# Kernel optimization log

Hardware: AMD Instinct MI355X
Metric: run time of the kernel (lower is better)

Reference implementation:

```python
import jax, jax.numpy as jnp
import numpy as np

NUM_HEADS = 16
FIELD_SIZE = 512
SIGMA = 3.0
EMB = 1024


def _causal_kernel_fft(G, sigma):
    # kernel[i] = exp(-|i - G//2| / sigma) for i < G//2, else 0; normalized
    i = np.arange(G)
    dist = np.abs(i - G // 2)
    kernel = np.where(i >= G // 2, 0.0, np.exp(-dist / sigma)).astype(np.float32)
    kernel = kernel / (kernel.sum() + 1e-8)
    return jnp.asarray(np.fft.rfft(kernel), dtype=jnp.complex64)


def setup_inputs() -> dict:
    key = jax.random.key(0)
    ks = jax.random.split(key, 9)
    B, N, D = 4, 4096, EMB
    s = 1.0 / np.sqrt(D)
    return {
        "x": jax.random.normal(ks[0], (B, N, D), dtype=jnp.float32),
        "q_w": jax.random.uniform(ks[1], (D, D), minval=-s, maxval=s, dtype=jnp.float32),
        "q_b": jnp.zeros((D,), jnp.float32),
        "k_w": jax.random.uniform(ks[2], (D, D), minval=-s, maxval=s, dtype=jnp.float32),
        "k_b": jnp.zeros((D,), jnp.float32),
        "v_w": jax.random.uniform(ks[3], (D, D), minval=-s, maxval=s, dtype=jnp.float32),
        "v_b": jnp.zeros((D,), jnp.float32),
        "out_w": jax.random.uniform(ks[4], (D, D), minval=-s, maxval=s, dtype=jnp.float32),
        "out_b": jnp.zeros((D,), jnp.float32),
    }


def reference(x, q_w, q_b, k_w, k_b, v_w, v_b, out_w, out_b):
    B, N, D = x.shape
    H, hd, G = NUM_HEADS, D // NUM_HEADS, FIELD_SIZE

    # projections (q is computed in the original but unused downstream)
    q = x @ q_w.T + q_b  # noqa: F841 (faithful to original)
    k = (x @ k_w.T + k_b).reshape(B, N, H, hd).transpose(0, 2, 1, 3)  # (B,H,N,hd)
    v = (x @ v_w.T + v_b).reshape(B, N, H, hd).transpose(0, 2, 1, 3)

    # map sequence positions -> field bins (same for all b, h)
    pos = jnp.arange(N, dtype=jnp.float32) / max(N - 1, 1) * (G - 1)
    field_idx = jnp.clip(pos.astype(jnp.int32), 0, G - 1)  # (N,)

    # weighted values by key magnitude
    k_mag = jnp.linalg.norm(k, axis=-1, keepdims=True)  # (B,H,N,1)
    wv = v * k_mag  # (B,H,N,hd)

    # scatter-add tokens into field bins (vectorized over B,H,hd)
    field = jax.ops.segment_sum(wv.transpose(2, 0, 1, 3), field_idx,
                                num_segments=G)  # (G,B,H,hd)
    field = field.transpose(1, 2, 0, 3)  # (B,H,G,hd)

    # causal convolution along the field via FFT (circular, as in original)
    kfft = _causal_kernel_fft(G, SIGMA)
    f_fft = jnp.fft.rfft(field, n=G, axis=2)
    conv = jnp.fft.irfft(f_fft * kfft[None, None, :, None], n=G, axis=2)

    # gather back to token positions
    out = conv[:, :, field_idx, :]  # (B,H,N,hd)
    out = out.transpose(0, 2, 1, 3).reshape(B, N, D)
    return out @ out_w.T + out_b
```

## Files before the change

kernel.cpp:

```cpp
#include <hip/hip_runtime.h>
#include <hip/hip_bf16.h>

#define NPOS 4096
#define DIM  1024
#define GSZ  512

#define GAS __attribute__((address_space(1)))
#define LAS __attribute__((address_space(3)))

typedef __attribute__((ext_vector_type(8))) short bf16x8;
typedef __attribute__((ext_vector_type(4))) float f32x4;

__device__ __forceinline__ void async_load16(const void* g, void* l) {
  __builtin_amdgcn_global_load_lds((const GAS void*)g, (LAS void*)l, 16, 0, 0);
}

__device__ __forceinline__ int fidx_of(int n) {
  return (int)(((float)n / 4095.0f) * 511.0f);
}

__device__ __forceinline__ float bf2f(unsigned short s) {
  union { unsigned u; float f; } v; v.u = ((unsigned)s) << 16; return v.f;
}

__global__ __launch_bounds__(256) void cast_f32_to_bf16(
    const float* __restrict__ src, __hip_bfloat16* __restrict__ dst, int n) {
  int i = (blockIdx.x * 256 + threadIdx.x) * 4;
  if (i < n) {
    float4 f = *(const float4*)(src + i);
    ushort4 o;
    __hip_bfloat16 t;
    t = __float2bfloat16(f.x); o.x = *(unsigned short*)&t;
    t = __float2bfloat16(f.y); o.y = *(unsigned short*)&t;
    t = __float2bfloat16(f.z); o.z = *(unsigned short*)&t;
    t = __float2bfloat16(f.w); o.w = *(unsigned short*)&t;
    *(ushort4*)(dst + i) = o;
  }
}

template<bool OUTBF16>
__global__ __launch_bounds__(256) void gemm_bt(
    const __hip_bfloat16* __restrict__ A,
    const __hip_bfloat16* __restrict__ B,
    const float* __restrict__ bias0, const float* __restrict__ bias1,
    void* __restrict__ Cv, int N) {
  const int K = 1024;
  __shared__ __align__(16) __hip_bfloat16 As[128 * 32];
  __shared__ __align__(16) __hip_bfloat16 Bs[128 * 32];
  const int tid = threadIdx.x;
  const int bm = blockIdx.x * 128, bn = blockIdx.y * 128;

  const int srow = tid >> 2;
  const int scol = (tid & 3) * 8;
  const __hip_bfloat16* ap0 = A + (size_t)(bm + srow) * K + scol;
  const __hip_bfloat16* ap1 = A + (size_t)(bm + srow + 64) * K + scol;
  const __hip_bfloat16* bp0 = B + (size_t)(bn + srow) * K + scol;
  const __hip_bfloat16* bp1 = B + (size_t)(bn + srow + 64) * K + scol;
  __hip_bfloat16* as0 = &As[srow * 32 + scol];
  __hip_bfloat16* as1 = &As[(srow + 64) * 32 + scol];
  __hip_bfloat16* bs0 = &Bs[srow * 32 + scol];
  __hip_bfloat16* bs1 = &Bs[(srow + 64) * 32 + scol];

  const int wave = tid >> 6, lane = tid & 63;
  const int wm = (wave >> 1) * 64, wn = (wave & 1) * 64;
  const int m16 = lane & 15, quad = lane >> 4;

  f32x4 acc[4][4];
#pragma unroll
  for (int i = 0; i < 4; i++)
#pragma unroll
    for (int j = 0; j < 4; j++) acc[i][j] = (f32x4)0.f;

  for (int k0 = 0; k0 < K; k0 += 32) {
    async_load16(ap0 + k0, as0);
    async_load16(ap1 + k0, as1);
    async_load16(bp0 + k0, bs0);
    async_load16(bp1 + k0, bs1);
    __syncthreads();
    bf16x8 af[4], bfr[4];
#pragma unroll
    for (int mt = 0; mt < 4; mt++)
      af[mt] = *(const bf16x8*)&As[(wm + mt * 16 + m16) * 32 + quad * 8];
#pragma unroll
    for (int nt = 0; nt < 4; nt++)
      bfr[nt] = *(const bf16x8*)&Bs[(wn + nt * 16 + m16) * 32 + quad * 8];
#pragma unroll
    for (int mt = 0; mt < 4; mt++)
#pragma unroll
      for (int nt = 0; nt < 4; nt++)
        acc[mt][nt] = __builtin_amdgcn_mfma_f32_16x16x32_bf16(af[mt], bfr[nt], acc[mt][nt], 0, 0, 0);
    __syncthreads();
  }

#pragma unroll
  for (int mt = 0; mt < 4; mt++) {
#pragma unroll
    for (int nt = 0; nt < 4; nt++) {
      int col = bn + wn + nt * 16 + m16;
      float bv = (col < 1024) ? bias0[col] : bias1[col - 1024];
#pragma unroll
      for (int r = 0; r < 4; r++) {
        int row = bm + wm + mt * 16 + quad * 4 + r;
        float v = acc[mt][nt][r] + bv;
        if (OUTBF16)
          ((__hip_bfloat16*)Cv)[(size_t)row * N + col] = __float2bfloat16(v);
        else
          ((float*)Cv)[(size_t)row * N + col] = v;
      }
    }
  }
}

__global__ __launch_bounds__(256) void wv_field_kernel(
    const __hip_bfloat16* __restrict__ KV, float* __restrict__ field) {
  const int b = blockIdx.x, g = blockIdx.y;
  int i0 = (g * 4095 + 510) / 511;
  while (i0 > 0 && fidx_of(i0 - 1) >= g) --i0;
  while (i0 < NPOS && fidx_of(i0) < g) ++i0;
  int i1;
  if (g == GSZ - 1) i1 = NPOS;
  else {
    i1 = ((g + 1) * 4095 + 510) / 511;
    while (i1 > 0 && fidx_of(i1 - 1) >= g + 1) --i1;
    while (i1 < NPOS && fidx_of(i1) < g + 1) ++i1;
  }
  int cnt = i1 - i0;
  if (cnt > 12) cnt = 12;
  __shared__ float km[12][16];
  const int tid = threadIdx.x;
  if (tid < cnt * 16) {
    int r = tid >> 4, h = tid & 15;
    const unsigned short* kp = (const unsigned short*)KV + (size_t)(b * NPOS + i0 + r) * 2048 + h * 64;
    float s = 0.f;
#pragma unroll
    for (int e = 0; e < 64; e += 8) {
      bf16x8 v = *(const bf16x8*)(kp + e);
#pragma unroll
      for (int q = 0; q < 8; ++q) { float f = bf2f((unsigned short)v[q]); s += f * f; }
    }
    km[r][h] = sqrtf(s);
  }
  __syncthreads();
  if (tid < 128) {
    int c0 = tid * 8, h = c0 >> 6;
    float acc[8] = {0.f, 0.f, 0.f, 0.f, 0.f, 0.f, 0.f, 0.f};
    for (int r = 0; r < cnt; ++r) {
      float w = km[r][h];
      bf16x8 v = *(const bf16x8*)((const unsigned short*)KV + (size_t)(b * NPOS + i0 + r) * 2048 + 1024 + c0);
#pragma unroll
      for (int q = 0; q < 8; ++q) acc[q] += w * bf2f((unsigned short)v[q]);
    }
    float4* fp = (float4*)(field + ((size_t)(b * GSZ + g)) * DIM + c0);
    fp[0] = make_float4(acc[0], acc[1], acc[2], acc[3]);
    fp[1] = make_float4(acc[4], acc[5], acc[6], acc[7]);
  }
}

__global__ __launch_bounds__(256) void conv_ema_kernel(
    const float* __restrict__ field, __hip_bfloat16* __restrict__ convb) {
  const int b = blockIdx.x, h = blockIdx.y;
  const int tid = threadIdx.x;
  const int c = tid & 63;
  const int chunk = blockIdx.z * 4 + (tid >> 6);
  const int n0 = chunk * 64;
  const float a = expf(-1.0f / 3.0f);
  const float w1 = 1.0f - a;
  const float* fb = field + (size_t)b * GSZ * DIM + h * 64 + c;
  float acc = 0.f;
#pragma unroll 4
  for (int n = n0 + 127; n >= n0 + 64; --n) {
    float f = fb[(size_t)((n + 257) & (GSZ - 1)) * DIM];
    acc = w1 * f + a * acc;
  }
#pragma unroll 4
  for (int n = n0 + 63; n >= n0; --n) {
    float f = fb[(size_t)((n + 257) & (GSZ - 1)) * DIM];
    acc = w1 * f + a * acc;
    convb[((size_t)(b * GSZ) + n) * DIM + h * 64 + c] = __float2bfloat16(acc);
  }
}

__global__ __launch_bounds__(256) void gather_out_kernel(
    const float* __restrict__ outc, float* __restrict__ out) {
  const int row = blockIdx.x;
  const int b = row >> 12, n = row & (NPOS - 1);
  const int g = fidx_of(n);
  const float4* src = (const float4*)(outc + ((size_t)(b * GSZ) + g) * DIM);
  float4* dst = (float4*)(out + (size_t)row * DIM);
  dst[threadIdx.x] = src[threadIdx.x];
}

extern "C" void kernel_launch(void* const* d_in, const int* in_sizes, int n_in,
                              void* d_out, int out_size, void* d_ws, size_t ws_size,
                              hipStream_t stream) {
  (void)in_sizes; (void)n_in; (void)out_size; (void)ws_size;
  const float* x     = (const float*)d_in[0];
  const float* k_w   = (const float*)d_in[3];
  const float* k_b   = (const float*)d_in[4];
  const float* v_w   = (const float*)d_in[5];
  const float* v_b   = (const float*)d_in[6];
  const float* out_w = (const float*)d_in[7];
  const float* out_b = (const float*)d_in[8];

  char* p = (char*)d_ws;
  __hip_bfloat16* xb    = (__hip_bfloat16*)p;
  float*          outc  = (float*)p;          p += (size_t)16384 * 1024 * 2;
  __hip_bfloat16* kvwb  = (__hip_bfloat16*)p; p += (size_t)2048 * 1024 * 2;
  __hip_bfloat16* outwb = (__hip_bfloat16*)p; p += (size_t)1024 * 1024 * 2;
  __hip_bfloat16* KV    = (__hip_bfloat16*)p; p += (size_t)16384 * 2048 * 2;
  float*          field = (float*)p;          p += (size_t)4 * 512 * 1024 * 4;
  __hip_bfloat16* convb = (__hip_bfloat16*)p;

  cast_f32_to_bf16<<<16384, 256, 0, stream>>>(x, xb, 16384 * 1024);
  cast_f32_to_bf16<<<1024, 256, 0, stream>>>(k_w, kvwb, 1024 * 1024);
  cast_f32_to_bf16<<<1024, 256, 0, stream>>>(v_w, kvwb + 1024 * 1024, 1024 * 1024);
  cast_f32_to_bf16<<<1024, 256, 0, stream>>>(out_w, outwb, 1024 * 1024);

  gemm_bt<true><<<dim3(128, 16), 256, 0, stream>>>(xb, kvwb, k_b, v_b, KV, 2048);

  wv_field_kernel<<<dim3(4, 512), 256, 0, stream>>>(KV, field);
  conv_ema_kernel<<<dim3(4, 16, 2), 256, 0, stream>>>(field, convb);

  gemm_bt<false><<<dim3(16, 8), 256, 0, stream>>>(convb, outwb, out_b, out_b, outc, 1024);
  gather_out_kernel<<<16384, 256, 0, stream>>>(outc, (float*)d_out);
}
```

Before: 296.1 us.

## Fuse output gather into output GEMM epilogue and merge cast kernels

The output projection GEMM now writes each field-bin result row straight to every token position mapped to that bin, which removes the intermediate fp32 buffer and the separate gather kernel. It uses a smaller 64-row M tile, giving 256 blocks instead of 128, for better occupancy. The four fp32-to-bf16 cast launches are merged into one kernel. The epilogue's scattered stores are only partially coalesced (16 consecutive floats per group), which may make the output write less efficient than the old float4 gather.

New measurement: 283.5 us. 4.3% less time.

```diff
diff --git a/kernel.cpp b/kernel.cpp
--- a/kernel.cpp
+++ b/kernel.cpp
@@ -23,27 +23,43 @@
   union { unsigned u; float f; } v; v.u = ((unsigned)s) << 16; return v.f;
 }
 
-__global__ __launch_bounds__(256) void cast_f32_to_bf16(
-    const float* __restrict__ src, __hip_bfloat16* __restrict__ dst, int n) {
-  int i = (blockIdx.x * 256 + threadIdx.x) * 4;
-  if (i < n) {
-    float4 f = *(const float4*)(src + i);
-    ushort4 o;
-    __hip_bfloat16 t;
-    t = __float2bfloat16(f.x); o.x = *(unsigned short*)&t;
-    t = __float2bfloat16(f.y); o.y = *(unsigned short*)&t;
-    t = __float2bfloat16(f.z); o.z = *(unsigned short*)&t;
-    t = __float2bfloat16(f.w); o.w = *(unsigned short*)&t;
-    *(ushort4*)(dst + i) = o;
-  }
-}
-
-template<bool OUTBF16>
+__device__ __forceinline__ void bin_range(int g, int& i0, int& i1) {
+  i0 = (g * 4095 + 510) / 511;
+  while (i0 > 0 && fidx_of(i0 - 1) >= g) --i0;
+  while (i0 < NPOS && fidx_of(i0) < g) ++i0;
+  if (g == GSZ - 1) { i1 = NPOS; return; }
+  i1 = ((g + 1) * 4095 + 510) / 511;
+  while (i1 > 0 && fidx_of(i1 - 1) >= g + 1) --i1;
+  while (i1 < NPOS && fidx_of(i1) < g + 1) ++i1;
+}
+
+__global__ __launch_bounds__(256) void cast_all(
+    const float* __restrict__ x, const float* __restrict__ kw,
+    const float* __restrict__ vw, const float* __restrict__ ow,
+    __hip_bfloat16* __restrict__ xb, __hip_bfloat16* __restrict__ kvwb,
+    __hip_bfloat16* __restrict__ outwb) {
+  int blk = blockIdx.x;
+  const float* src; __hip_bfloat16* dst; int off;
+  if (blk < 16384)      { src = x;  dst = xb;              off = blk; }
+  else if (blk < 17408) { src = kw; dst = kvwb;            off = blk - 16384; }
+  else if (blk < 18432) { src = vw; dst = kvwb + 1048576;  off = blk - 17408; }
+  else                  { src = ow; dst = outwb;           off = blk - 18432; }
+  int i = (off * 256 + threadIdx.x) * 4;
+  float4 f = *(const float4*)(src + i);
+  ushort4 o;
+  __hip_bfloat16 t;
+  t = __float2bfloat16(f.x); o.x = *(unsigned short*)&t;
+  t = __float2bfloat16(f.y); o.y = *(unsigned short*)&t;
+  t = __float2bfloat16(f.z); o.z = *(unsigned short*)&t;
+  t = __float2bfloat16(f.w); o.w = *(unsigned short*)&t;
+  *(ushort4*)(dst + i) = o;
+}
+
 __global__ __launch_bounds__(256) void gemm_bt(
     const __hip_bfloat16* __restrict__ A,
     const __hip_bfloat16* __restrict__ B,
     const float* __restrict__ bias0, const float* __restrict__ bias1,
-    void* __restrict__ Cv, int N) {
+    __hip_bfloat16* __restrict__ C, int N) {
   const int K = 1024;
   __shared__ __align__(16) __hip_bfloat16 As[128 * 32];
   __shared__ __align__(16) __hip_bfloat16 Bs[128 * 32];
@@ -101,11 +117,84 @@
 #pragma unroll
       for (int r = 0; r < 4; r++) {
         int row = bm + wm + mt * 16 + quad * 4 + r;
-        float v = acc[mt][nt][r] + bv;
-        if (OUTBF16)
-          ((__hip_bfloat16*)Cv)[(size_t)row * N + col] = __float2bfloat16(v);
-        else
-          ((float*)Cv)[(size_t)row * N + col] = v;
+        C[(size_t)row * N + col] = __float2bfloat16(acc[mt][nt][r] + bv);
+      }
+    }
+  }
+}
+
+__global__ __launch_bounds__(256) void gemm_out_bcast(
+    const __hip_bfloat16* __restrict__ A,
+    const __hip_bfloat16* __restrict__ B,
+    const float* __restrict__ bias,
+    float* __restrict__ out) {
+  const int K = 1024;
+  __shared__ __align__(16) __hip_bfloat16 As[64 * 32];
+  __shared__ __align__(16) __hip_bfloat16 Bs[128 * 32];
+  const int tid = threadIdx.x;
+  const int bm = blockIdx.x * 64, bn = blockIdx.y * 128;
+
+  const int srow = tid >> 2;
+  const int scol = (tid & 3) * 8;
+  const __hip_bfloat16* ap0 = A + (size_t)(bm + srow) * K + scol;
+  const __hip_bfloat16* bp0 = B + (size_t)(bn + srow) * K + scol;
+  const __hip_bfloat16* bp1 = B + (size_t)(bn + srow + 64) * K + scol;
+  __hip_bfloat16* as0 = &As[srow * 32 + scol];
+  __hip_bfloat16* bs0 = &Bs[srow * 32 + scol];
+  __hip_bfloat16* bs1 = &Bs[(srow + 64) * 32 + scol];
+
+  const int wave = tid >> 6, lane = tid & 63;
+  const int wm = (wave >> 1) * 32, wn = (wave & 1) * 64;
+  const int m16 = lane & 15, quad = lane >> 4;
+
+  f32x4 acc[2][4];
+#pragma unroll
+  for (int i = 0; i < 2; i++)
+#pragma unroll
+    for (int j = 0; j < 4; j++) acc[i][j] = (f32x4)0.f;
+
+  for (int k0 = 0; k0 < K; k0 += 32) {
+    async_load16(ap0 + k0, as0);
+    async_load16(bp0 + k0, bs0);
+    async_load16(bp1 + k0, bs1);
+    __syncthreads();
+    bf16x8 af[2], bfr[4];
+#pragma unroll
+    for (int mt = 0; mt < 2; mt++)
+      af[mt] = *(const bf16x8*)&As[(wm + mt * 16 + m16) * 32 + quad * 8];
+#pragma unroll
+    for (int nt = 0; nt < 4; nt++)
+      bfr[nt] = *(const bf16x8*)&Bs[(wn + nt * 16 + m16) * 32 + quad * 8];
+#pragma unroll
+    for (int mt = 0; mt < 2; mt++)
+#pragma unroll
+      for (int nt = 0; nt < 4; nt++)
+        acc[mt][nt] = __builtin_amdgcn_mfma_f32_16x16x32_bf16(af[mt], bfr[nt], acc[mt][nt], 0, 0, 0);
+    __syncthreads();
+  }
+
+  float bv[4];
+#pragma unroll
+  for (int nt = 0; nt < 4; nt++) bv[nt] = bias[bn + wn + nt * 16 + m16];
+
+#pragma unroll
+  for (int mt = 0; mt < 2; mt++) {
+#pragma unroll
+    for (int r = 0; r < 4; r++) {
+      int row = bm + wm + mt * 16 + quad * 4 + r;
+      int b = row >> 9, g = row & (GSZ - 1);
+      int i0, i1;
+      bin_range(g, i0, i1);
+      float v0 = acc[mt][0][r] + bv[0];
+      float v1 = acc[mt][1][r] + bv[1];
+      float v2 = acc[mt][2][r] + bv[2];
+      float v3 = acc[mt][3][r] + bv[3];
+      for (int n = i0; n < i1; ++n) {
+        float* orow = out + ((size_t)(b * NPOS + n)) * DIM + bn + wn + m16;
+        orow[0]  = v0;
+        orow[16] = v1;
+        orow[32] = v2;
+        orow[48] = v3;
       }
     }
   }
@@ -114,16 +203,8 @@
 __global__ __launch_bounds__(256) void wv_field_kernel(
     const __hip_bfloat16* __restrict__ KV, float* __restrict__ field) {
   const int b = blockIdx.x, g = blockIdx.y;
-  int i0 = (g * 4095 + 510) / 511;
-  while (i0 > 0 && fidx_of(i0 - 1) >= g) --i0;
-  while (i0 < NPOS && fidx_of(i0) < g) ++i0;
-  int i1;
-  if (g == GSZ - 1) i1 = NPOS;
-  else {
-    i1 = ((g + 1) * 4095 + 510) / 511;
-    while (i1 > 0 && fidx_of(i1 - 1) >= g + 1) --i1;
-    while (i1 < NPOS && fidx_of(i1) < g + 1) ++i1;
-  }
+  int i0, i1;
+  bin_range(g, i0, i1);
   int cnt = i1 - i0;
   if (cnt > 12) cnt = 12;
   __shared__ float km[12][16];
@@ -180,16 +261,6 @@
   }
 }
 
-__global__ __launch_bounds__(256) void gather_out_kernel(
-    const float* __restrict__ outc, float* __restrict__ out) {
-  const int row = blockIdx.x;
-  const int b = row >> 12, n = row & (NPOS - 1);
-  const int g = fidx_of(n);
-  const float4* src = (const float4*)(outc + ((size_t)(b * GSZ) + g) * DIM);
-  float4* dst = (float4*)(out + (size_t)row * DIM);
-  dst[threadIdx.x] = src[threadIdx.x];
-}
-
 extern "C" void kernel_launch(void* const* d_in, const int* in_sizes, int n_in,
                               void* d_out, int out_size, void* d_ws, size_t ws_size,
                               hipStream_t stream) {
@@ -203,24 +274,19 @@
   const float* out_b = (const float*)d_in[8];
 
   char* p = (char*)d_ws;
-  __hip_bfloat16* xb    = (__hip_bfloat16*)p;
-  float*          outc  = (float*)p;          p += (size_t)16384 * 1024 * 2;
+  __hip_bfloat16* xb    = (__hip_bfloat16*)p; p += (size_t)16384 * 1024 * 2;
   __hip_bfloat16* kvwb  = (__hip_bfloat16*)p; p += (size_t)2048 * 1024 * 2;
   __hip_bfloat16* outwb = (__hip_bfloat16*)p; p += (size_t)1024 * 1024 * 2;
   __hip_bfloat16* KV    = (__hip_bfloat16*)p; p += (size_t)16384 * 2048 * 2;
   float*          field = (float*)p;          p += (size_t)4 * 512 * 1024 * 4;
   __hip_bfloat16* convb = (__hip_bfloat16*)p;
 
-  cast_f32_to_bf16<<<16384, 256, 0, stream>>>(x, xb, 16384 * 1024);
-  cast_f32_to_bf16<<<1024, 256, 0, stream>>>(k_w, kvwb, 1024 * 1024);
-  cast_f32_to_bf16<<<1024, 256, 0, stream>>>(v_w, kvwb + 1024 * 1024, 1024 * 1024);
-  cast_f32_to_bf16<<<1024, 256, 0, stream>>>(out_w, outwb, 1024 * 1024);
-
-  gemm_bt<true><<<dim3(128, 16), 256, 0, stream>>>(xb, kvwb, k_b, v_b, KV, 2048);
+  cast_all<<<19456, 256, 0, stream>>>(x, k_w, v_w, out_w, xb, kvwb, outwb);
+
+  gemm_bt<<<dim3(128, 16), 256, 0, stream>>>(xb, kvwb, k_b, v_b, KV, 2048);
 
   wv_field_kernel<<<dim3(4, 512), 256, 0, stream>>>(KV, field);
   conv_ema_kernel<<<dim3(4, 16, 2), 256, 0, stream>>>(field, convb);
 
-  gemm_bt<false><<<dim3(16, 8), 256, 0, stream>>>(convb, outwb, out_b, out_b, outc, 1024);
-  gather_out_kernel<<<16384, 256, 0, stream>>>(outc, (float*)d_out);
-}
+  gemm_out_bcast<<<dim3(32, 8), 256, 0, stream>>>(convb, outwb, out_b, (float*)d_out);
+}
```
